# Performance work log

Hardware: AMD Instinct MI355X
Metric: run time of the kernel (lower is better)

Reference implementation:

```python
import jax, jax.numpy as jnp
import numpy as np
import math

B = 200        # graphs
NPG = 512      # nodes per graph
EPG = 8192     # edges per graph (avg degree 16)
E = B * EPG
FIN = 11
H = 128


def setup_inputs() -> dict:
    key = jax.random.key(0)
    ks = jax.random.split(key, 16)
    g = jnp.arange(E, dtype=jnp.int32) // EPG  # graph id per edge
    edge_src = g * NPG + jax.random.randint(ks[0], (E,), 0, NPG, dtype=jnp.int32)
    edge_dst = g * NPG + jax.random.randint(ks[1], (E,), 0, NPG, dtype=jnp.int32)
    x = jax.random.normal(ks[2], (B * NPG, FIN), dtype=jnp.float32)

    def w(k, shape):
        return jax.random.normal(k, shape, dtype=jnp.float32) * 0.1

    return dict(
        x=x, edge_src=edge_src, edge_dst=edge_dst,
        num_graphs=B, nodes_per_graph=NPG,
        Wrel1=w(ks[3], (H, FIN)), Wroot1=w(ks[4], (H, FIN)), b1=jnp.zeros((H,), jnp.float32), pw1=w(ks[5], (H,)),
        Wrel2=w(ks[6], (H, H)), Wroot2=w(ks[7], (H, H)), b2=jnp.zeros((H,), jnp.float32), pw2=w(ks[8], (H,)),
        Wrel3=w(ks[9], (H, H)), Wroot3=w(ks[10], (H, H)), b3=jnp.zeros((H,), jnp.float32), pw3=w(ks[11], (H,)),
        Wl1=w(ks[12], (512, 256)), bl1=jnp.zeros((512,), jnp.float32),
        Wl2=w(ks[13], (64, 512)), bl2=jnp.zeros((64,), jnp.float32),
        Wl3=w(ks[14], (1, 64)), bl3=jnp.zeros((1,), jnp.float32),
    )


def graph_conv(x, src, dst, emask, Wrel, Wroot, b):
    # PyG GraphConv (aggr='add'): lin_rel(sum_j x_j) + lin_root(x)
    msg = x[src] * emask[:, None]                    # [E, F] gather + edge mask
    agg = jax.ops.segment_sum(msg, dst, num_segments=x.shape[0])
    return agg @ Wrel.T + b + x @ Wroot.T


def topk_pool(x, src, dst, emask, w, ratio, B):
    # PyG TopKPooling: score = tanh((x . w)/||w||), keep top ceil(ratio*N) per graph
    N = x.shape[0] // B
    k = int(math.ceil(ratio * N))
    score = jnp.tanh((x @ w) / jnp.linalg.norm(w))   # [B*N]
    _, idx = jax.lax.top_k(score.reshape(B, N), k)   # local indices per graph
    perm = (idx + (jnp.arange(B, dtype=idx.dtype) * N)[:, None]).reshape(-1)  # [B*k]
    xk = x[perm] * score[perm][:, None]
    # old node id -> new node id (or -1 if dropped); reindex edges, mask invalid
    newid = jnp.full((B * N,), -1, dtype=jnp.int32).at[perm].set(jnp.arange(B * k, dtype=jnp.int32))
    ns, nd = newid[src], newid[dst]
    keep = emask * (ns >= 0) * (nd >= 0)
    return xk, jnp.maximum(ns, 0), jnp.maximum(nd, 0), keep.astype(x.dtype)


def readout(x, B):
    # cat([global_max_pool, global_mean_pool]); uniform graph sizes -> reshape
    xr = x.reshape(B, -1, x.shape[-1])
    return jnp.concatenate([xr.max(axis=1), xr.mean(axis=1)], axis=-1)


def reference(x, edge_src, edge_dst, num_graphs, nodes_per_graph,
              Wrel1, Wroot1, b1, pw1, Wrel2, Wroot2, b2, pw2,
              Wrel3, Wroot3, b3, pw3, Wl1, bl1, Wl2, bl2, Wl3, bl3):
    Bg = num_graphs
    src, dst = edge_src, edge_dst
    emask = jnp.ones(src.shape, x.dtype)
    h = jax.nn.relu(graph_conv(x, src, dst, emask, Wrel1, Wroot1, b1))
    h, src, dst, emask = topk_pool(h, src, dst, emask, pw1, 0.5, Bg)
    x1 = readout(h, Bg)
    h = jax.nn.relu(graph_conv(h, src, dst, emask, Wrel2, Wroot2, b2))
    h, src, dst, emask = topk_pool(h, src, dst, emask, pw2, 0.8, Bg)
    x2 = readout(h, Bg)
    h = jax.nn.relu(graph_conv(h, src, dst, emask, Wrel3, Wroot3, b3))
    h, src, dst, emask = topk_pool(h, src, dst, emask, pw3, 0.8, Bg)
    x3 = readout(h, Bg)
    z = x1 + x2 + x3
    z = jax.nn.relu(z @ Wl1.T + bl1)   # dropout p=0.7 is identity in eval mode
    z = jax.nn.relu(z @ Wl2.T + bl2)
    return z @ Wl3.T + bl3             # [B, 1]
```

## Files before the change

kernel.cpp:

```cpp
#include <hip/hip_runtime.h>
#include <math.h>

#define BG   200
#define NPGc 512
#define EPGc 8192
#define NE   (BG*EPGc)
#define N0   (BG*NPGc)
#define FINc 11
#define Hc   128
#define K1c  256
#define K2c  205
#define K3c  164
#define N1   (BG*K1c)
#define N2   (BG*K2c)
#define N3   (BG*K3c)

typedef float f32x4 __attribute__((ext_vector_type(4)));
typedef short s16x8 __attribute__((ext_vector_type(8)));

#define PL ((size_t)N1*Hc)
#define PA ((size_t)N0*32)

__device__ inline unsigned short bf16_rne(float v){
  unsigned u = __float_as_uint(v);
  unsigned r = u + 0x7FFFu + ((u >> 16) & 1u);
  return (unsigned short)(r >> 16);
}
__device__ inline float bf16_f32(unsigned short h){
  return __uint_as_float(((unsigned)h) << 16);
}
__device__ inline void split3(float v, unsigned short& r0, unsigned short& r1,
                              unsigned short& r2){
  r0 = bf16_rne(v); float v1 = v - bf16_f32(r0);
  r1 = bf16_rne(v1); float v2 = v1 - bf16_f32(r1);
  r2 = bf16_rne(v2);
}

__device__ inline size_t flIdx(int row, int k){
  return ((size_t)(row >> 4))*2048 + (size_t)(k >> 3)*128
       + (size_t)(row & 15)*8 + (size_t)(k & 7);
}
__device__ inline size_t flIdx32(int row, int k){
  return ((size_t)(row >> 4))*512 + (size_t)(k >> 3)*128
       + (size_t)(row & 15)*8 + (size_t)(k & 7);
}

__launch_bounds__(512)
__global__ void k_csr(const int* __restrict__ esrc, const int* __restrict__ edst,
                      int* __restrict__ deg, int* __restrict__ rowptr,
                      int* __restrict__ csr){
  __shared__ int ed[EPGc];
  __shared__ int cnt[NPGc];
  __shared__ int sc[NPGc];
  int g = blockIdx.x, t = threadIdx.x;
  cnt[t] = 0;
  __syncthreads();
  int gb = g*EPGc;
  for (int i=t; i<EPGc; i+=512){
    int dl = edst[gb+i] & (NPGc-1);
    ed[i] = dl;
    atomicAdd(&cnt[dl], 1);
  }
  __syncthreads();
  int d = cnt[t];
  sc[t] = d;
  __syncthreads();
  for (int o=1;o<NPGc;o<<=1){
    int v = (t>=o) ? sc[t-o] : 0;
    __syncthreads();
    sc[t] += v;
    __syncthreads();
  }
  deg[g*NPGc+t]    = d;
  rowptr[g*NPGc+t] = gb + sc[t] - d;
  cnt[t] = sc[t] - d;
  __syncthreads();
  for (int i=t; i<EPGc; i+=512){
    int p = atomicAdd(&cnt[ed[i]], 1);
    csr[gb+p] = esrc[gb+i];
  }
}

__global__ void k_prep(const float* __restrict__ Wl1, const float* __restrict__ Wl2,
                       float* __restrict__ Wl1T, float* __restrict__ Wl2T){
  int idx = blockIdx.x*256 + threadIdx.x;
  if (idx < 256*512){
    int f = idx >> 9, t = idx & 511;
    Wl1T[idx] = Wl1[t*256 + f];
  }
  if (idx < 512*64){
    int f = idx >> 6, t = idx & 63;
    Wl2T[idx] = Wl2[t*512 + f];
  }
}

__global__ void k_prepw(const float* __restrict__ Wrel2, const float* __restrict__ Wroot2,
                        const float* __restrict__ Wrel3, const float* __restrict__ Wroot3,
                        unsigned short* __restrict__ Wsp){
  int t = blockIdx.x*256 + threadIdx.x;
  if (t >= 65536) return;
  int L = t >> 15, p = (t >> 14) & 1, ck = t & 16383;
  int c = ck >> 7, k = ck & 127;
  const float* W = L ? (p ? Wroot3 : Wrel3) : (p ? Wroot2 : Wrel2);
  unsigned short r0, r1, r2;
  split3(W[c*128 + k], r0, r1, r2);
  unsigned short* base = Wsp + (size_t)((L*2+p)*3)*16384;
  size_t fl = flIdx(c, k);
  base[fl]          = r0;
  base[16384 + fl]  = r1;
  base[32768 + fl]  = r2;
}

__global__ void k_prepw1(const float* __restrict__ Wrel1, const float* __restrict__ Wroot1,
                         unsigned short* __restrict__ W1S){
  int t = blockIdx.x*256 + threadIdx.x;
  if (t >= 4096) return;
  int c = t >> 5, k = t & 31;
  float v = (k < 11) ? Wrel1[c*11 + k] : (k < 22 ? Wroot1[c*11 + (k-11)] : 0.f);
  unsigned short r0, r1, r2;
  split3(v, r0, r1, r2);
  size_t fl = flIdx32(c, k);
  W1S[fl]        = r0;
  W1S[4096 + fl] = r1;
  W1S[8192 + fl] = r2;
}

__global__ void k_pwnorm(const float* __restrict__ pw1, const float* __restrict__ pw2,
                         const float* __restrict__ pw3, float* __restrict__ norms){
  __shared__ float s[384];
  int t = threadIdx.x;
  int which = t >> 7, idx = t & 127;
  float v = (which==0) ? pw1[idx] : (which==1 ? pw2[idx] : pw3[idx]);
  s[t] = v*v;
  __syncthreads();
  if (t < 3){
    float sum = 0.f;
    for (int i=0;i<128;i++) sum += s[t*128+i];
    norms[t] = sqrtf(sum);
  }
}

__global__ void k_agg1(const float* __restrict__ x, const int* __restrict__ csr,
                       const int* __restrict__ rowptr, const int* __restrict__ deg,
                       float* __restrict__ agg1){
  int bid = (int)((blockIdx.x & 7)*3200 + (blockIdx.x >> 3));
  int d = bid*4 + (threadIdx.x >> 6);
  if (d >= N0) return;
  int lane = threadIdx.x & 63;
  int slot = lane >> 4, f = lane & 15;
  int rs = rowptr[d], dg = deg[d];
  float a0 = 0.f, a1 = 0.f;
  for (int base=0; base<dg; base+=64){
    int e = base + lane;
    int s = 0;
    if (e < dg) s = csr[rs+e];
    int cnt = min(64, dg-base);
    for (int jj=0; jj<cnt; jj+=8){
      int s0 = __shfl(s, (jj + slot) & 63);
      int s1 = __shfl(s, (jj + 4 + slot) & 63);
      if (jj + slot < cnt && f < FINc)     a0 += x[s0*FINc + f];
      if (jj + 4 + slot < cnt && f < FINc) a1 += x[s1*FINc + f];
    }
  }
  a0 += a1;
  a0 += __shfl_xor(a0, 16);
  a0 += __shfl_xor(a0, 32);
  if (slot == 0 && f < FINc) agg1[d*FINc + f] = a0;
}

__global__ void k_splitA(const float* __restrict__ x, const float* __restrict__ agg1,
                         unsigned short* __restrict__ AS){
  int gid = blockIdx.x*256 + threadIdx.x;
  int row = gid >> 4, j = gid & 15;
  int k0 = j*2, k1 = k0 + 1;
  float v0 = (k0 < 11) ? agg1[row*11 + k0] : (k0 < 22 ? x[row*11 + (k0-11)] : 0.f);
  float v1 = (k1 < 11) ? agg1[row*11 + k1] : (k1 < 22 ? x[row*11 + (k1-11)] : 0.f);
  unsigned short a0,a1,a2,b0,b1,b2;
  split3(v0, a0, a1, a2);
  split3(v1, b0, b1, b2);
  size_t fl = flIdx32(row, k0);
  *(unsigned*)&AS[fl]        = (unsigned)a0 | ((unsigned)b0 << 16);
  *(unsigned*)&AS[PA + fl]   = (unsigned)a1 | ((unsigned)b1 << 16);
  *(unsigned*)&AS[2*PA + fl] = (unsigned)a2 | ((unsigned)b2 << 16);
}

__launch_bounds__(256)
__global__ void k_conv1m(const unsigned short* __restrict__ AS,
                         const unsigned short* __restrict__ W1S,
                         const float* __restrict__ bias, const float* __restrict__ pw,
                         const float* __restrict__ norm_p,
                         float* __restrict__ hout, float* __restrict__ score, int M){
  __shared__ float scds[64][2];
  int tid = threadIdx.x;
  int w = tid >> 6, l = tid & 63;
  int wm = w >> 1, wn = w & 1;
  int lr = l & 15, lk = l >> 4;
  int m0 = blockIdx.x * 64;

  f32x4 acc[2][4];
  #pragma unroll
  for (int mi=0;mi<2;mi++)
    #pragma unroll
    for (int ni=0;ni<4;ni++) acc[mi][ni] = (f32x4){0.f,0.f,0.f,0.f};

  s16x8 af[3][2], bf[3][4];
  #pragma unroll
  for (int mi=0; mi<2; mi++){
    int tile = (m0 + wm*32 + mi*16) >> 4;
    size_t idx = (size_t)tile*512 + (size_t)lk*128 + (size_t)lr*8;
    af[0][mi] = *(const s16x8*)&AS[idx];
    af[1][mi] = *(const s16x8*)&AS[PA + idx];
    af[2][mi] = *(const s16x8*)&AS[2*PA + idx];
  }
  #pragma unroll
  for (int ni=0; ni<4; ni++){
    int ct = wn*4 + ni;
    size_t idx = (size_t)ct*512 + (size_t)lk*128 + (size_t)lr*8;
    bf[0][ni] = *(const s16x8*)&W1S[idx];
    bf[1][ni] = *(const s16x8*)&W1S[4096 + idx];
    bf[2][ni] = *(const s16x8*)&W1S[8192 + idx];
  }
  #define TRM(sa,sb) \
    _Pragma("unroll") \
    for (int ni=0; ni<4; ni++){ \
      _Pragma("unroll") \
      for (int mi=0; mi<2; mi++){ \
        acc[mi][ni] = __builtin_amdgcn_mfma_f32_16x16x32_bf16(af[sa][mi], bf[sb][ni], acc[mi][ni], 0,0,0); \
      } \
    }
  TRM(0,0) TRM(0,1) TRM(1,0) TRM(1,1) TRM(0,2) TRM(2,0)
  #undef TRM

  float nrm = *norm_p;
  float pwv[4], biasv[4];
  #pragma unroll
  for (int ni=0;ni<4;ni++){
    int col = wn*64 + ni*16 + lr;
    pwv[ni] = pw[col]; biasv[ni] = bias[col];
  }
  #pragma unroll
  for (int mi=0; mi<2; mi++){
    #pragma unroll
    for (int reg=0; reg<4; reg++){
      int rl = wm*32 + mi*16 + lk*4 + reg;
      int row = m0 + rl;
      float hv[4]; float sc = 0.f;
      #pragma unroll
      for (int ni=0; ni<4; ni++){
        hv[ni] = fmaxf(acc[mi][ni][reg] + biasv[ni], 0.f);
        sc += hv[ni]*pwv[ni];
      }
      if (row < M){
        #pragma unroll
        for (int ni=0; ni<4; ni++)
          hout[(size_t)row*Hc + wn*64 + ni*16 + lr] = hv[ni];
      }
      sc += __shfl_xor(sc,1); sc += __shfl_xor(sc,2);
      sc += __shfl_xor(sc,4); sc += __shfl_xor(sc,8);
      if (lr == 0) scds[rl][wn] = sc;
    }
  }
  __syncthreads();
  if (tid < 64){
    int row = m0 + tid;
    if (row < M) score[row] = tanhf((scds[tid][0] + scds[tid][1]) / nrm);
  }
}

template<int N, int K, int NP2>
__global__ void k_topk(const float* __restrict__ score, int* __restrict__ newid,
                       int* __restrict__ perm){
  __shared__ float sv[NP2];
  __shared__ int   si[NP2];
  int g = blockIdx.x, t = threadIdx.x;
  sv[t] = (t < N) ? score[g*N + t] : -INFINITY;
  si[t] = t;
  __syncthreads();
  for (int k=2;k<=NP2;k<<=1){
    for (int j=k>>1;j>0;j>>=1){
      int p = t ^ j;
      if (p > t){
        float va = sv[t], vb = sv[p];
        int   ia = si[t], ib = si[p];
        bool good = (va > vb) || (va == vb && ia < ib);
        bool up   = ((t & k) == 0);
        if (good != up){ sv[t]=vb; si[t]=ib; sv[p]=va; si[p]=ia; }
      }
      __syncthreads();
    }
  }
  if (t < N) newid[g*N + t] = -1;
  __syncthreads();
  if (t < K){
    int old = si[t];
    newid[g*N + old] = g*K + t;
    perm[g*K + t]    = g*N + old;
  }
}

__launch_bounds__(1024)
__global__ void k_gatherR(const float* __restrict__ h, const float* __restrict__ score,
                          const int* __restrict__ perm, float* __restrict__ hp,
                          unsigned short* __restrict__ hpS, float* __restrict__ z,
                          int kk, int doSplit){
  __shared__ float smx[8][Hc];
  __shared__ float ssm[8][Hc];
  int g = blockIdx.x;
  int rg = threadIdx.x >> 7, j = threadIdx.x & 127;
  float mx = -INFINITY, sm = 0.f;
  for (int r=rg; r<kk; r+=8){
    int m = g*kk + r;
    int p = perm[m];
    float v = h[(size_t)p*Hc + j] * score[p];
    hp[(size_t)m*Hc + j] = v;
    float vn = __shfl_xor(v, 1);
    if (doSplit && !(j & 1)){
      unsigned short a0,a1,a2,b0,b1,b2;
      split3(v,  a0, a1, a2);
      split3(vn, b0, b1, b2);
      size_t fl = flIdx(m, j);
      *(unsigned*)&hpS[fl]        = (unsigned)a0 | ((unsigned)b0 << 16);
      *(unsigned*)&hpS[PL + fl]   = (unsigned)a1 | ((unsigned)b1 << 16);
      *(unsigned*)&hpS[2*PL + fl] = (unsigned)a2 | ((unsigned)b2 << 16);
    }
    mx = fmaxf(mx, v); sm += v;
  }
  smx[rg][j] = mx; ssm[rg][j] = sm;
  __syncthreads();
  if (rg == 0){
    #pragma unroll
    for (int u=1; u<8; u++){
      mx = fmaxf(mx, smx[u][j]); sm += ssm[u][j];
    }
    z[g*256 + j]       += mx;
    z[g*256 + 128 + j] += sm / (float)kk;
  }
}

__global__ void k_compose(const int* __restrict__ map1, const int* __restrict__ newid2,
                          int* __restrict__ map2, const int* __restrict__ perm1,
                          const int* __restrict__ perm2, int* __restrict__ orig3){
  int o = blockIdx.x*256 + threadIdx.x;
  if (o < N0){ int m = map1[o]; map2[o] = (m>=0) ? newid2[m] : -1; }
  if (o < N2){ orig3[o] = perm1[perm2[o]]; }
}

__global__ void k_aggHs(const int* __restrict__ orig, const int* __restrict__ map,
                        const float* __restrict__ hp,
                        const int* __restrict__ csr, const int* __restrict__ rowptr,
                        const int* __restrict__ deg, unsigned short* __restrict__ aggS,
                        int M){
  int cpx = gridDim.x >> 3;
  int bid = (int)((blockIdx.x & 7)*cpx + (blockIdx.x >> 3));
  int m = bid*4 + (threadIdx.x>>6);
  int lane = threadIdx.x & 63;
  if (m >= M) return;
  int d = orig[m];
  int rs = rowptr[d], dg = deg[d];
  int half = lane >> 5, cl = lane & 31;
  f32x4 acc[4];
  #pragma unroll
  for (int u=0;u<4;u++) acc[u] = (f32x4){0.f,0.f,0.f,0.f};
  for (int base=0; base<dg; base+=64){
    int e = base + lane;
    int ns = -1;
    if (e < dg){ int s = csr[rs+e]; ns = map[s]; }
    int cnt = min(64, dg-base);
    for (int jj=0; jj<cnt; jj+=8){
      #pragma unroll
      for (int u=0; u<4; u++){
        int ei = jj + u*2 + half;
        int nsj = __shfl(ns, ei & 63);
        if (ei < cnt && nsj >= 0){
          acc[u] += *(const f32x4*)(hp + (size_t)nsj*Hc + cl*4);
        }
      }
    }
  }
  f32x4 s4 = (acc[0]+acc[1]) + (acc[2]+acc[3]);
  #pragma unroll
  for (int i=0;i<4;i++) s4[i] += __shfl_xor(s4[i], 32);
  float e0 = __shfl(s4[0], lane>>1);
  float e1 = __shfl(s4[1], lane>>1);
  float e2 = __shfl(s4[2], lane>>1);
  float e3 = __shfl(s4[3], lane>>1);
  float cx = (lane&1) ? e2 : e0;
  float cy = (lane&1) ? e3 : e1;
  unsigned short x0,x1,x2,y0,y1,y2;
  split3(cx, x0, x1, x2);
  split3(cy, y0, y1, y2);
  size_t fl = flIdx(m, 2*lane);
  *(unsigned*)&aggS[fl]        = (unsigned)x0 | ((unsigned)y0 << 16);
  *(unsigned*)&aggS[PL + fl]   = (unsigned)x1 | ((unsigned)y1 << 16);
  *(unsigned*)&aggS[2*PL + fl] = (unsigned)x2 | ((unsigned)y2 << 16);
}

__launch_bounds__(256)
__global__ void k_convH(const unsigned short* __restrict__ A0s,
                        const unsigned short* __restrict__ A1s,
                        const unsigned short* __restrict__ Wsp,
                        const float* __restrict__ bias, const float* __restrict__ pw,
                        const float* __restrict__ norm_p,
                        float* __restrict__ hout, float* __restrict__ score, int M){
  __shared__ float scds[64][2];
  int tid = threadIdx.x;
  int w = tid >> 6, l = tid & 63;
  int wm = w >> 1, wn = w & 1;
  int lr = l & 15, lk = l >> 4;
  int m0 = blockIdx.x * 64;

  f32x4 acc[2][4];
  #pragma unroll
  for (int mi=0;mi<2;mi++)
    #pragma unroll
    for (int ni=0;ni<4;ni++) acc[mi][ni] = (f32x4){0.f,0.f,0.f,0.f};

  #pragma unroll
  for (int kc=0; kc<4; kc++){
    #pragma unroll
    for (int p=0; p<2; p++){
      const unsigned short* As = p ? A1s : A0s;
      const unsigned short* Wp = Wsp + (size_t)p*3*16384;
      s16x8 af[3][2], bf[3][4];
      #pragma unroll
      for (int mi=0; mi<2; mi++){
        int tile = (m0 + wm*32 + mi*16) >> 4;
        size_t idx = (size_t)tile*2048 + (size_t)(kc*4+lk)*128 + (size_t)lr*8;
        af[0][mi] = *(const s16x8*)&As[idx];
        af[1][mi] = *(const s16x8*)&As[PL + idx];
        af[2][mi] = *(const s16x8*)&As[2*PL + idx];
      }
      #pragma unroll
      for (int ni=0; ni<4; ni++){
        int ct = wn*4 + ni;
        size_t idx = (size_t)ct*2048 + (size_t)(kc*4+lk)*128 + (size_t)lr*8;
        bf[0][ni] = *(const s16x8*)&Wp[idx];
        bf[1][ni] = *(const s16x8*)&Wp[16384 + idx];
        bf[2][ni] = *(const s16x8*)&Wp[32768 + idx];
      }
      #define TRM(sa,sb) \
        _Pragma("unroll") \
        for (int ni=0; ni<4; ni++){ \
          _Pragma("unroll") \
          for (int mi=0; mi<2; mi++){ \
            acc[mi][ni] = __builtin_amdgcn_mfma_f32_16x16x32_bf16(af[sa][mi], bf[sb][ni], acc[mi][ni], 0,0,0); \
          } \
        }
      TRM(0,0) TRM(0,1) TRM(1,0) TRM(1,1) TRM(0,2) TRM(2,0)
      #undef TRM
    }
  }

  float nrm = *norm_p;
  float pwv[4], biasv[4];
  #pragma unroll
  for (int ni=0;ni<4;ni++){
    int col = wn*64 + ni*16 + lr;
    pwv[ni] = pw[col]; biasv[ni] = bias[col];
  }
  #pragma unroll
  for (int mi=0; mi<2; mi++){
    #pragma unroll
    for (int reg=0; reg<4; reg++){
      int rl = wm*32 + mi*16 + lk*4 + reg;
      int row = m0 + rl;
      float hv[4]; float sc = 0.f;
      #pragma unroll
      for (int ni=0; ni<4; ni++){
        hv[ni] = fmaxf(acc[mi][ni][reg] + biasv[ni], 0.f);
        sc += hv[ni]*pwv[ni];
      }
      if (row < M){
        #pragma unroll
        for (int ni=0; ni<4; ni++)
          hout[(size_t)row*Hc + wn*64 + ni*16 + lr] = hv[ni];
      }
      sc += __shfl_xor(sc,1); sc += __shfl_xor(sc,2);
      sc += __shfl_xor(sc,4); sc += __shfl_xor(sc,8);
      if (lr == 0) scds[rl][wn] = sc;
    }
  }
  __syncthreads();
  if (tid < 64){
    int row = m0 + tid;
    if (row < M) score[row] = tanhf((scds[tid][0] + scds[tid][1]) / nrm);
  }
}

__launch_bounds__(512)
__global__ void k_mlp(const float* __restrict__ z,
                      const float* __restrict__ Wl1T, const float* __restrict__ bl1,
                      const float* __restrict__ Wl2T, const float* __restrict__ bl2,
                      const float* __restrict__ Wl3, const float* __restrict__ bl3,
                      float* __restrict__ out){
  __shared__ float zs[256];
  __shared__ float u1[512];
  int g = blockIdx.x, t = threadIdx.x;
  if (t < 256) zs[t] = z[g*256 + t];
  __syncthreads();
  {
    float acc = bl1[t];
    #pragma unroll 8
    for (int f=0; f<256; f++) acc = fmaf(zs[f], Wl1T[f*512 + t], acc);
    u1[t] = fmaxf(acc, 0.f);
  }
  __syncthreads();
  if (t < 64){
    float acc = bl2[t];
    #pragma unroll 8
    for (int f=0; f<512; f++) acc = fmaf(u1[f], Wl2T[f*64 + t], acc);
    float v = fmaxf(acc, 0.f) * Wl3[t];
    for (int o=32;o>0;o>>=1) v += __shfl_xor(v, o);
    if (t == 0) out[g] = v + bl3[0];
  }
}

extern "C" void kernel_launch(void* const* d_in, const int* in_sizes, int n_in,
                              void* d_out, int out_size, void* d_ws, size_t ws_size,
                              hipStream_t stream){
  const float* x     = (const float*)d_in[0];
  const int*   esrc  = (const int*)d_in[1];
  const int*   edst  = (const int*)d_in[2];
  const float* Wrel1 = (const float*)d_in[5];
  const float* Wroot1= (const float*)d_in[6];
  const float* b1    = (const float*)d_in[7];
  const float* pw1   = (const float*)d_in[8];
  const float* Wrel2 = (const float*)d_in[9];
  const float* Wroot2= (const float*)d_in[10];
  const float* b2    = (const float*)d_in[11];
  const float* pw2   = (const float*)d_in[12];
  const float* Wrel3 = (const float*)d_in[13];
  const float* Wroot3= (const float*)d_in[14];
  const float* b3    = (const float*)d_in[15];
  const float* pw3   = (const float*)d_in[16];
  const float* Wl1   = (const float*)d_in[17];
  const float* bl1   = (const float*)d_in[18];
  const float* Wl2   = (const float*)d_in[19];
  const float* bl2   = (const float*)d_in[20];
  const float* Wl3   = (const float*)d_in[21];
  const float* bl3   = (const float*)d_in[22];
  float* out = (float*)d_out;

  char* ws = (char*)d_ws;
  size_t off = 0;
  auto alloc = [&](size_t elems)->void*{
    void* p = ws + off;
    off += ((elems*4 + 255)/256)*256;
    return p;
  };
  int*   deg    = (int*)alloc(N0);
  int*   rowptr = (int*)alloc(N0);
  int*   csr    = (int*)alloc(NE);
  int*   map1   = (int*)alloc(N0);
  int*   newid2 = (int*)alloc(N1);
  int*   map2   = (int*)alloc(N0);
  int*   perm1  = (int*)alloc(N1);
  int*   perm2  = (int*)alloc(N2);
  int*   perm3  = (int*)alloc(N3);
  int*   orig3  = (int*)alloc(N2);
  float* score1 = (float*)alloc(N0);
  float* score2 = (float*)alloc(N1);
  float* score3 = (float*)alloc(N2);
  float* agg1   = (float*)alloc((size_t)N0*FINc);
  float* Wl1T   = (float*)alloc(256*512);
  float* Wl2T   = (float*)alloc(512*64);
  unsigned short* Wsp = (unsigned short*)alloc(98304);
  unsigned short* W1S = (unsigned short*)alloc(6144);
  float* norms  = (float*)alloc(3);
  float* bigA   = (float*)alloc((size_t)N0*Hc);
  float* hB     = (float*)alloc((size_t)N1*Hc);
  float* hpA    = (float*)alloc((size_t)N1*Hc);
  unsigned short* hpS = (unsigned short*)alloc((size_t)3*N1*Hc/2);
  float* z      = (float*)alloc(BG*256);

  float* h1   = bigA;
  unsigned short* aggS = (unsigned short*)bigA;
  unsigned short* a1S  = hpS;
  float* h2   = hB;
  float* h3   = hB;

  hipMemsetAsync(z, 0, BG*256*sizeof(float), stream);

  k_csr    <<<BG, 512, 0, stream>>>(esrc, edst, deg, rowptr, csr);
  k_prep   <<<512, 256, 0, stream>>>(Wl1, Wl2, Wl1T, Wl2T);
  k_prepw  <<<256, 256, 0, stream>>>(Wrel2, Wroot2, Wrel3, Wroot3, Wsp);
  k_prepw1 <<<16, 256, 0, stream>>>(Wrel1, Wroot1, W1S);
  k_pwnorm <<<1, 384, 0, stream>>>(pw1, pw2, pw3, norms);

  k_agg1   <<<N0/4, 256, 0, stream>>>(x, csr, rowptr, deg, agg1);
  k_splitA <<<N0*16/256, 256, 0, stream>>>(x, agg1, a1S);
  k_conv1m <<<N0/64, 256, 0, stream>>>(a1S, W1S, b1, pw1, norms+0, h1, score1, N0);
  k_topk<NPGc, K1c, 512><<<BG, 512, 0, stream>>>(score1, map1, perm1);
  k_gatherR<<<BG, 1024, 0, stream>>>(h1, score1, perm1, hpA, hpS, z, K1c, 1);

  k_aggHs  <<<N1/4, 256, 0, stream>>>(perm1, map1, hpA, csr, rowptr, deg, aggS, N1);
  k_convH  <<<N1/64, 256, 0, stream>>>(aggS, hpS, Wsp, b2, pw2, norms+1, h2, score2, N1);
  k_topk<K1c, K2c, 256><<<BG, 256, 0, stream>>>(score2, newid2, perm2);
  k_compose<<<N0/256, 256, 0, stream>>>(map1, newid2, map2, perm1, perm2, orig3);
  k_gatherR<<<BG, 1024, 0, stream>>>(h2, score2, perm2, hpA, hpS, z, K2c, 1);

  k_aggHs  <<<10256, 256, 0, stream>>>(orig3, map2, hpA, csr, rowptr, deg, aggS, N2);
  k_convH  <<<(N2+63)/64, 256, 0, stream>>>(aggS, hpS, Wsp + 98304, b3, pw3, norms+2, h3, score3, N2);
  k_topk<K2c, K3c, 256><<<BG, 256, 0, stream>>>(score3, newid2, perm3);
  k_gatherR<<<BG, 1024, 0, stream>>>(h3, score3, perm3, hpA, hpS, z, K3c, 0);

  k_mlp<<<BG, 512, 0, stream>>>(z, Wl1T, bl1, Wl2T, bl2, Wl3, bl3, out);
}
```

Baseline: 323.0 us.

## Fuse prep kernels and restructure aggregation as per-graph LDS-resident blocks

Merges the four weight-prep kernels and the z memset into one launch. Fuses layer-1 aggregation with the bf16 split. Folds map composition into top-k. Replaces the per-node aggregation kernels with one block per graph that stages that graph's features (x, or pooled hidden up to 256x128 floats, about 128KB) in shared memory and gathers neighbours from LDS instead of global memory. This removes several launches and global gather traffic, but only 200 blocks run and the LDS footprint limits occupancy, leaving parallelism much lower than the previous many-block launches.

Result: slower. 469.1 us (+45.2%).

```diff
diff --git a/kernel.cpp b/kernel.cpp
--- a/kernel.cpp
+++ b/kernel.cpp
@@ -81,8 +81,15 @@
   }
 }
 
-__global__ void k_prep(const float* __restrict__ Wl1, const float* __restrict__ Wl2,
-                       float* __restrict__ Wl1T, float* __restrict__ Wl2T){
+__global__ void k_prepall(const float* __restrict__ Wrel1, const float* __restrict__ Wroot1,
+                          const float* __restrict__ Wrel2, const float* __restrict__ Wroot2,
+                          const float* __restrict__ Wrel3, const float* __restrict__ Wroot3,
+                          const float* __restrict__ Wl1, const float* __restrict__ Wl2,
+                          const float* __restrict__ pw1, const float* __restrict__ pw2,
+                          const float* __restrict__ pw3,
+                          float* __restrict__ Wl1T, float* __restrict__ Wl2T,
+                          unsigned short* __restrict__ Wsp, unsigned short* __restrict__ W1S,
+                          float* __restrict__ z, float* __restrict__ norms){
   int idx = blockIdx.x*256 + threadIdx.x;
   if (idx < 256*512){
     int f = idx >> 9, t = idx & 511;
@@ -92,96 +99,88 @@
     int f = idx >> 6, t = idx & 63;
     Wl2T[idx] = Wl2[t*512 + f];
   }
-}
-
-__global__ void k_prepw(const float* __restrict__ Wrel2, const float* __restrict__ Wroot2,
-                        const float* __restrict__ Wrel3, const float* __restrict__ Wroot3,
-                        unsigned short* __restrict__ Wsp){
-  int t = blockIdx.x*256 + threadIdx.x;
-  if (t >= 65536) return;
-  int L = t >> 15, p = (t >> 14) & 1, ck = t & 16383;
-  int c = ck >> 7, k = ck & 127;
-  const float* W = L ? (p ? Wroot3 : Wrel3) : (p ? Wroot2 : Wrel2);
-  unsigned short r0, r1, r2;
-  split3(W[c*128 + k], r0, r1, r2);
-  unsigned short* base = Wsp + (size_t)((L*2+p)*3)*16384;
-  size_t fl = flIdx(c, k);
-  base[fl]          = r0;
-  base[16384 + fl]  = r1;
-  base[32768 + fl]  = r2;
-}
-
-__global__ void k_prepw1(const float* __restrict__ Wrel1, const float* __restrict__ Wroot1,
-                         unsigned short* __restrict__ W1S){
-  int t = blockIdx.x*256 + threadIdx.x;
-  if (t >= 4096) return;
-  int c = t >> 5, k = t & 31;
-  float v = (k < 11) ? Wrel1[c*11 + k] : (k < 22 ? Wroot1[c*11 + (k-11)] : 0.f);
-  unsigned short r0, r1, r2;
-  split3(v, r0, r1, r2);
-  size_t fl = flIdx32(c, k);
-  W1S[fl]        = r0;
-  W1S[4096 + fl] = r1;
-  W1S[8192 + fl] = r2;
-}
-
-__global__ void k_pwnorm(const float* __restrict__ pw1, const float* __restrict__ pw2,
-                         const float* __restrict__ pw3, float* __restrict__ norms){
-  __shared__ float s[384];
-  int t = threadIdx.x;
-  int which = t >> 7, idx = t & 127;
-  float v = (which==0) ? pw1[idx] : (which==1 ? pw2[idx] : pw3[idx]);
-  s[t] = v*v;
-  __syncthreads();
-  if (t < 3){
-    float sum = 0.f;
-    for (int i=0;i<128;i++) sum += s[t*128+i];
-    norms[t] = sqrtf(sum);
-  }
-}
-
-__global__ void k_agg1(const float* __restrict__ x, const int* __restrict__ csr,
-                       const int* __restrict__ rowptr, const int* __restrict__ deg,
-                       float* __restrict__ agg1){
-  int bid = (int)((blockIdx.x & 7)*3200 + (blockIdx.x >> 3));
-  int d = bid*4 + (threadIdx.x >> 6);
-  if (d >= N0) return;
-  int lane = threadIdx.x & 63;
+  if (idx < 65536){
+    int L = idx >> 15, p = (idx >> 14) & 1, ck = idx & 16383;
+    int c = ck >> 7, k = ck & 127;
+    const float* W = L ? (p ? Wroot3 : Wrel3) : (p ? Wroot2 : Wrel2);
+    unsigned short r0, r1, r2;
+    split3(W[c*128 + k], r0, r1, r2);
+    unsigned short* base = Wsp + (size_t)((L*2+p)*3)*16384;
+    size_t fl = flIdx(c, k);
+    base[fl]          = r0;
+    base[16384 + fl]  = r1;
+    base[32768 + fl]  = r2;
+  }
+  if (idx < 4096){
+    int c = idx >> 5, k = idx & 31;
+    float v = (k < 11) ? Wrel1[c*11 + k] : (k < 22 ? Wroot1[c*11 + (k-11)] : 0.f);
+    unsigned short r0, r1, r2;
+    split3(v, r0, r1, r2);
+    size_t fl = flIdx32(c, k);
+    W1S[fl]        = r0;
+    W1S[4096 + fl] = r1;
+    W1S[8192 + fl] = r2;
+  }
+  if (idx < BG*256) z[idx] = 0.f;
+  if (blockIdx.x == 511){
+    int w = threadIdx.x >> 6, lane = threadIdx.x & 63;
+    if (w < 3){
+      const float* pw = (w==0) ? pw1 : (w==1 ? pw2 : pw3);
+      float v0 = pw[lane], v1 = pw[64+lane];
+      float ss = v0*v0 + v1*v1;
+      for (int o=32;o>0;o>>=1) ss += __shfl_xor(ss, o);
+      if (lane == 0) norms[w] = sqrtf(ss);
+    }
+  }
+}
+
+__launch_bounds__(512)
+__global__ void k_agg1f(const float* __restrict__ x, const int* __restrict__ csr,
+                        const int* __restrict__ rowptr, const int* __restrict__ deg,
+                        unsigned short* __restrict__ AS){
+  __shared__ float xs[NPGc*FINc];
+  int g = blockIdx.x, t = threadIdx.x;
+  int gb = g*NPGc;
+  const float* xg = x + (size_t)gb*FINc;
+  for (int i=t; i<NPGc*FINc/4; i+=512)
+    ((f32x4*)xs)[i] = ((const f32x4*)xg)[i];
+  __syncthreads();
+  int w = t >> 6, lane = t & 63;
   int slot = lane >> 4, f = lane & 15;
-  int rs = rowptr[d], dg = deg[d];
-  float a0 = 0.f, a1 = 0.f;
-  for (int base=0; base<dg; base+=64){
-    int e = base + lane;
-    int s = 0;
-    if (e < dg) s = csr[rs+e];
-    int cnt = min(64, dg-base);
-    for (int jj=0; jj<cnt; jj+=8){
-      int s0 = __shfl(s, (jj + slot) & 63);
-      int s1 = __shfl(s, (jj + 4 + slot) & 63);
-      if (jj + slot < cnt && f < FINc)     a0 += x[s0*FINc + f];
-      if (jj + 4 + slot < cnt && f < FINc) a1 += x[s1*FINc + f];
-    }
-  }
-  a0 += a1;
-  a0 += __shfl_xor(a0, 16);
-  a0 += __shfl_xor(a0, 32);
-  if (slot == 0 && f < FINc) agg1[d*FINc + f] = a0;
-}
-
-__global__ void k_splitA(const float* __restrict__ x, const float* __restrict__ agg1,
-                         unsigned short* __restrict__ AS){
-  int gid = blockIdx.x*256 + threadIdx.x;
-  int row = gid >> 4, j = gid & 15;
-  int k0 = j*2, k1 = k0 + 1;
-  float v0 = (k0 < 11) ? agg1[row*11 + k0] : (k0 < 22 ? x[row*11 + (k0-11)] : 0.f);
-  float v1 = (k1 < 11) ? agg1[row*11 + k1] : (k1 < 22 ? x[row*11 + (k1-11)] : 0.f);
-  unsigned short a0,a1,a2,b0,b1,b2;
-  split3(v0, a0, a1, a2);
-  split3(v1, b0, b1, b2);
-  size_t fl = flIdx32(row, k0);
-  *(unsigned*)&AS[fl]        = (unsigned)a0 | ((unsigned)b0 << 16);
-  *(unsigned*)&AS[PA + fl]   = (unsigned)a1 | ((unsigned)b1 << 16);
-  *(unsigned*)&AS[2*PA + fl] = (unsigned)a2 | ((unsigned)b2 << 16);
+  for (int r = w; r < NPGc; r += 8){
+    int d = gb + r;
+    int rs = rowptr[d], dg = deg[d];
+    float a0 = 0.f, a1 = 0.f;
+    for (int base=0; base<dg; base+=64){
+      int e = base + lane;
+      int s = 0;
+      if (e < dg) s = csr[rs+e] & (NPGc-1);
+      int cnt = min(64, dg-base);
+      for (int jj=0; jj<cnt; jj+=8){
+        int s0 = __shfl(s, (jj + slot) & 63);
+        int s1 = __shfl(s, (jj + 4 + slot) & 63);
+        if (jj + slot < cnt && f < FINc)     a0 += xs[s0*FINc + f];
+        if (jj + 4 + slot < cnt && f < FINc) a1 += xs[s1*FINc + f];
+      }
+    }
+    a0 += a1;
+    a0 += __shfl_xor(a0, 16);
+    a0 += __shfl_xor(a0, 32);
+    int k0 = 2*lane, k1 = k0 + 1;
+    float s0 = __shfl(a0, k0 & 63);
+    float s1 = __shfl(a0, k1 & 63);
+    if (lane < 16){
+      float v0 = (k0 < 11) ? s0 : ((k0 < 22) ? xs[r*FINc + k0 - 11] : 0.f);
+      float v1 = (k1 < 11) ? s1 : ((k1 < 22) ? xs[r*FINc + k1 - 11] : 0.f);
+      unsigned short a_0,a_1,a_2,b_0,b_1,b_2;
+      split3(v0, a_0, a_1, a_2);
+      split3(v1, b_0, b_1, b_2);
+      size_t fl = flIdx32(d, k0);
+      *(unsigned*)&AS[fl]        = (unsigned)a_0 | ((unsigned)b_0 << 16);
+      *(unsigned*)&AS[PA + fl]   = (unsigned)a_1 | ((unsigned)b_1 << 16);
+      *(unsigned*)&AS[2*PA + fl] = (unsigned)a_2 | ((unsigned)b_2 << 16);
+    }
+  }
 }
 
 __launch_bounds__(256)
@@ -269,9 +268,12 @@
 
 template<int N, int K, int NP2>
 __global__ void k_topk(const float* __restrict__ score, int* __restrict__ newid,
-                       int* __restrict__ perm){
+                       int* __restrict__ perm,
+                       const int* __restrict__ map1In, int* __restrict__ map2Out,
+                       const int* __restrict__ origPrev, int* __restrict__ origOut){
   __shared__ float sv[NP2];
   __shared__ int   si[NP2];
+  __shared__ int   nid[N];
   int g = blockIdx.x, t = threadIdx.x;
   sv[t] = (t < N) ? score[g*N + t] : -INFINITY;
   si[t] = t;
@@ -289,12 +291,20 @@
       __syncthreads();
     }
   }
-  if (t < N) newid[g*N + t] = -1;
-  __syncthreads();
+  if (t < N) nid[si[t]] = (t < K) ? t : -1;
+  __syncthreads();
+  if (t < N) newid[g*N + t] = (nid[t] >= 0) ? g*K + nid[t] : -1;
   if (t < K){
     int old = si[t];
-    newid[g*N + old] = g*K + t;
-    perm[g*K + t]    = g*N + old;
+    perm[g*K + t] = g*N + old;
+    if (origOut) origOut[g*K + t] = origPrev[g*N + old];
+  }
+  if (map2Out){
+    for (int o = t; o < NPGc; o += NP2){
+      int m = map1In[g*NPGc + o];
+      int r = (m >= 0) ? nid[m - g*N] : -1;
+      map2Out[g*NPGc + o] = (r >= 0) ? g*K + r : -1;
+    }
   }
 }
 
@@ -337,62 +347,52 @@
   }
 }
 
-__global__ void k_compose(const int* __restrict__ map1, const int* __restrict__ newid2,
-                          int* __restrict__ map2, const int* __restrict__ perm1,
-                          const int* __restrict__ perm2, int* __restrict__ orig3){
-  int o = blockIdx.x*256 + threadIdx.x;
-  if (o < N0){ int m = map1[o]; map2[o] = (m>=0) ? newid2[m] : -1; }
-  if (o < N2){ orig3[o] = perm1[perm2[o]]; }
-}
-
-__global__ void k_aggHs(const int* __restrict__ orig, const int* __restrict__ map,
-                        const float* __restrict__ hp,
-                        const int* __restrict__ csr, const int* __restrict__ rowptr,
-                        const int* __restrict__ deg, unsigned short* __restrict__ aggS,
-                        int M){
-  int cpx = gridDim.x >> 3;
-  int bid = (int)((blockIdx.x & 7)*cpx + (blockIdx.x >> 3));
-  int m = bid*4 + (threadIdx.x>>6);
-  int lane = threadIdx.x & 63;
-  if (m >= M) return;
-  int d = orig[m];
-  int rs = rowptr[d], dg = deg[d];
-  int half = lane >> 5, cl = lane & 31;
-  f32x4 acc[4];
-  #pragma unroll
-  for (int u=0;u<4;u++) acc[u] = (f32x4){0.f,0.f,0.f,0.f};
-  for (int base=0; base<dg; base+=64){
-    int e = base + lane;
-    int ns = -1;
-    if (e < dg){ int s = csr[rs+e]; ns = map[s]; }
-    int cnt = min(64, dg-base);
-    for (int jj=0; jj<cnt; jj+=8){
-      #pragma unroll
-      for (int u=0; u<4; u++){
-        int ei = jj + u*2 + half;
-        int nsj = __shfl(ns, ei & 63);
-        if (ei < cnt && nsj >= 0){
-          acc[u] += *(const f32x4*)(hp + (size_t)nsj*Hc + cl*4);
+__launch_bounds__(512)
+__global__ void k_aggL(const int* __restrict__ orig, const int* __restrict__ map,
+                       const float* __restrict__ hp,
+                       const int* __restrict__ csr, const int* __restrict__ rowptr,
+                       const int* __restrict__ deg, unsigned short* __restrict__ aggS,
+                       int K){
+  __shared__ float hps[K1c*Hc];
+  __shared__ int   ml[NPGc];
+  int g = blockIdx.x, t = threadIdx.x;
+  const float* hpg = hp + (size_t)g*K*Hc;
+  int nv = K*Hc/4;
+  for (int i=t; i<nv; i+=512)
+    ((f32x4*)hps)[i] = ((const f32x4*)hpg)[i];
+  if (t < NPGc){
+    int m = map[g*NPGc + t];
+    ml[t] = (m >= 0) ? (m - g*K) : -1;
+  }
+  __syncthreads();
+  int w = t >> 6, lane = t & 63;
+  for (int r = w; r < K; r += 8){
+    int mg = g*K + r;
+    int dOrig = orig[mg];
+    int rs = rowptr[dOrig], dg = deg[dOrig];
+    float ax = 0.f, ay = 0.f;
+    for (int base=0; base<dg; base+=64){
+      int e = base + lane;
+      int s = 0;
+      if (e < dg) s = csr[rs+e] & (NPGc-1);
+      int cnt = min(64, dg-base);
+      for (int jj=0; jj<cnt; jj++){
+        int sj = __shfl(s, jj);
+        int ns = ml[sj];
+        if (ns >= 0){
+          float2 v = ((const float2*)(hps + (size_t)ns*Hc))[lane];
+          ax += v.x; ay += v.y;
         }
       }
     }
-  }
-  f32x4 s4 = (acc[0]+acc[1]) + (acc[2]+acc[3]);
-  #pragma unroll
-  for (int i=0;i<4;i++) s4[i] += __shfl_xor(s4[i], 32);
-  float e0 = __shfl(s4[0], lane>>1);
-  float e1 = __shfl(s4[1], lane>>1);
-  float e2 = __shfl(s4[2], lane>>1);
-  float e3 = __shfl(s4[3], lane>>1);
-  float cx = (lane&1) ? e2 : e0;
-  float cy = (lane&1) ? e3 : e1;
-  unsigned short x0,x1,x2,y0,y1,y2;
-  split3(cx, x0, x1, x2);
-  split3(cy, y0, y1, y2);
-  size_t fl = flIdx(m, 2*lane);
-  *(unsigned*)&aggS[fl]        = (unsigned)x0 | ((unsigned)y0 << 16);
-  *(unsigned*)&aggS[PL + fl]   = (unsigned)x1 | ((unsigned)y1 << 16);
-  *(unsigned*)&aggS[2*PL + fl] = (unsigned)x2 | ((unsigned)y2 << 16);
+    unsigned short x0,x1,x2,y0,y1,y2;
+    split3(ax, x0, x1, x2);
+    split3(ay, y0, y1, y2);
+    size_t fl = flIdx(mg, 2*lane);
+    *(unsigned*)&aggS[fl]        = (unsigned)x0 | ((unsigned)y0 << 16);
+    *(unsigned*)&aggS[PL + fl]   = (unsigned)x1 | ((unsigned)y1 << 16);
+    *(unsigned*)&aggS[2*PL + fl] = (unsigned)x2 | ((unsigned)y2 << 16);
+  }
 }
 
 __launch_bounds__(256)
@@ -561,7 +561,6 @@
   float* score1 = (float*)alloc(N0);
   float* score2 = (float*)alloc(N1);
   float* score3 = (float*)alloc(N2);
-  float* agg1   = (float*)alloc((size_t)N0*FINc);
   float* Wl1T   = (float*)alloc(256*512);
   float* Wl2T   = (float*)alloc(512*64);
   unsigned short* Wsp = (unsigned short*)alloc(98304);
@@ -579,29 +578,27 @@
   float* h2   = hB;
   float* h3   = hB;
 
-  hipMemsetAsync(z, 0, BG*256*sizeof(float), stream);
-
+  k_prepall<<<512, 256, 0, stream>>>(Wrel1, Wroot1, Wrel2, Wroot2, Wrel3, Wroot3,
+                                     Wl1, Wl2, pw1, pw2, pw3,
+                                     Wl1T, Wl2T, Wsp, W1S, z, norms);
   k_csr    <<<BG, 512, 0, stream>>>(esrc, edst, deg, rowptr, csr);
-  k_prep   <<<512, 256, 0, stream>>>(Wl1, Wl2, Wl1T, Wl2T);
-  k_prepw  <<<256, 256, 0, stream>>>(Wrel2, Wroot2, Wrel3, Wroot3, Wsp);
-  k_prepw1 <<<16, 256, 0, stream>>>(Wrel1, Wroot1, W1S);
-  k_pwnorm <<<1, 384, 0, stream>>>(pw1, pw2, pw3, norms);
-
-  k_agg1   <<<N0/4, 256, 0, stream>>>(x, csr, rowptr, deg, agg1);
-  k_splitA <<<N0*16/256, 256, 0, stream>>>(x, agg1, a1S);
+
+  k_agg1f  <<<BG, 512, 0, stream>>>(x, csr, rowptr, deg, a1S);
   k_conv1m <<<N0/64, 256, 0, stream>>>(a1S, W1S, b1, pw1, norms+0, h1, score1, N0);
-  k_topk<NPGc, K1c, 512><<<BG, 512, 0, stream>>>(score1, map1, perm1);
+  k_topk<NPGc, K1c, 512><<<BG, 512, 0, stream>>>(score1, map1, perm1,
+                                                 nullptr, nullptr, nullptr, nullptr);
   k_gatherR<<<BG, 1024, 0, stream>>>(h1, score1, perm1, hpA, hpS, z, K1c, 1);
 
-  k_aggHs  <<<N1/4, 256, 0, stream>>>(perm1, map1, hpA, csr, rowptr, deg, aggS, N1);
+  k_aggL   <<<BG, 512, 0, stream>>>(perm1, map1, hpA, csr, rowptr, deg, aggS, K1c);
   k_convH  <<<N1/64, 256, 0, stream>>>(aggS, hpS, Wsp, b2, pw2, norms+1, h2, score2, N1);
-  k_topk<K1c, K2c, 256><<<BG, 256, 0, stream>>>(score2, newid2, perm2);
-  k_compose<<<N0/256, 256, 0, stream>>>(map1, newid2, map2, perm1, perm2, orig3);
+  k_topk<K1c, K2c, 256><<<BG, 256, 0, stream>>>(score2, newid2, perm2,
+                                                map1, map2, perm1, orig3);
   k_gatherR<<<BG, 1024, 0, stream>>>(h2, score2, perm2, hpA, hpS, z, K2c, 1);
 
-  k_aggHs  <<<10256, 256, 0, stream>>>(orig3, map2, hpA, csr, rowptr, deg, aggS, N2);
+  k_aggL   <<<BG, 512, 0, stream>>>(orig3, map2, hpA, csr, rowptr, deg, aggS, K2c);
   k_convH  <<<(N2+63)/64, 256, 0, stream>>>(aggS, hpS, Wsp + 98304, b3, pw3, norms+2, h3, score3, N2);
-  k_topk<K2c, K3c, 256><<<BG, 256, 0, stream>>>(score3, newid2, perm3);
+  k_topk<K2c, K3c, 256><<<BG, 256, 0, stream>>>(score3, newid2, perm3,
+                                                nullptr, nullptr, nullptr, nullptr);
   k_gatherR<<<BG, 1024, 0, stream>>>(h3, score3, perm3, hpA, hpS, z, K3c, 0);
 
   k_mlp<<<BG, 512, 0, stream>>>(z, Wl1T, bl1, Wl2T, bl2, Wl3, bl3, out);
```
